# Kernel optimization log

Hardware: AMD Instinct MI355X
Metric: run time of the kernel (lower is better)

## Reference

```python
import jax, jax.numpy as jnp
import numpy as np

TEMPERATURE = 1.0


def setup_inputs() -> dict:
    key = jax.random.key(0)
    k1, k2, k3, k4, k5 = jax.random.split(key, 5)
    B, S, F = 4, 2048, 2048   # batch, seq, in_features
    E, r, O = 8, 16, 2048     # experts, lora rank, out_features
    x = jax.random.normal(k1, (B, S, F), dtype=jnp.float32)
    protos = jax.random.normal(k2, (E, F), dtype=jnp.float32)
    protos = protos / (jnp.linalg.norm(protos, axis=-1, keepdims=True) + 1e-8)  # unit prototypes (top singular vecs)
    A_stack = jax.random.normal(k3, (E, r, F), dtype=jnp.float32) * 0.02
    B_stack = jax.random.normal(k4, (E, O, r), dtype=jnp.float32) * 0.02
    scales = jax.random.uniform(k5, (E,), dtype=jnp.float32)
    return {"x": x, "prototypes": protos, "A_stack": A_stack,
            "B_stack": B_stack, "scales": scales, "top_k": 2}


def reference(x, prototypes, A_stack, B_stack, scales, top_k):
    B, S, F = x.shape
    tok = x.reshape(-1, F)                       # [t, F]
    t = tok.shape[0]
    # 1) |cosine| similarity to prototypes (protos are unit norm)
    sim = jnp.abs(tok @ prototypes.T)            # [t, E]
    # 2) top-k selection, softmax over selected (others -inf)
    top_v, idx = jax.lax.top_k(sim, top_k)       # [t, k]
    full_score = jnp.full(sim.shape, -jnp.inf, dtype=sim.dtype)
    full_score = full_score.at[jnp.arange(t)[:, None], idx].set(top_v)
    coeff = jax.nn.softmax(full_score / TEMPERATURE, axis=1)   # [t, E]
    # 3-5) per-expert LoRA deltas, scaled, then coefficient-weighted sum
    z = jnp.einsum('tf,erf->ter', tok, A_stack)                # [t, E, r]
    y = jnp.einsum('ter,eor->teo', z, B_stack)                 # [t, E, O]
    y = y * scales[None, :, None]
    delta_flat = jnp.einsum('te,teo->to', coeff, y)            # [t, O]
    # 6) dropout is identity in eval mode
    return delta_flat.reshape(B, S, -1)
```

## Files before the change

### kernel.cpp

```cpp
#include <hip/hip_runtime.h>
#include <hip/hip_bf16.h>

typedef unsigned short u16;
typedef __bf16 bf16x8 __attribute__((ext_vector_type(8)));
typedef float f32x4 __attribute__((ext_vector_type(4)));

#define T_TOTAL 8192
#define F_DIM   2048
#define E_NUM   8
#define R_RANK  16
#define ER_DIM  128
#define O_DIM   2048

__device__ __forceinline__ u16 f2bf(float f) {
  return __builtin_bit_cast(u16, (__bf16)f);
}

__global__ __launch_bounds__(256) void prep_kernel(
    const float* __restrict__ A, const float* __restrict__ Bst,
    u16* __restrict__ Abf, u16* __restrict__ BbfT) {
  const int i = blockIdx.x * 256 + threadIdx.x;
  Abf[i] = f2bf(A[i]);
  const int o = i >> 7, er = i & 127, e = er >> 4, j = er & 15;
  BbfT[i] = f2bf(Bst[e * (O_DIM * R_RANK) + o * R_RANK + j]);
}

__global__ __launch_bounds__(256) void gemm1_kernel(
    const float* __restrict__ x, const float* __restrict__ protos,
    const float* __restrict__ scales, const u16* __restrict__ Abf,
    u16* __restrict__ zc) {
  __shared__ u16 xs[16 * 136];
  __shared__ u16 as_[128 * 136];
  __shared__ float pk[8 * 128];
  __shared__ float sim_lds[16][8];
  __shared__ float w_lds[16][8];

  const int tid  = threadIdx.x;
  const int t0   = blockIdx.x * 16;
  const int row  = tid >> 4;
  const int seg  = tid & 15;
  const int lane = tid & 63;
  const int wave = tid >> 6;
  const int g    = lane >> 4;
  const int lm   = lane & 15;

  float sacc[E_NUM];
#pragma unroll
  for (int e = 0; e < E_NUM; ++e) sacc[e] = 0.f;

  const f32x4 z4 = {0.f, 0.f, 0.f, 0.f};
  f32x4 acc[2];
  acc[0] = z4; acc[1] = z4;

  for (int kt = 0; kt < F_DIM / 128; ++kt) {
    const int kb = kt * 128;
    __syncthreads();

    f32x4 xv[2];
    const float* xp = x + (size_t)(t0 + row) * F_DIM + kb + seg * 4;
    xv[0] = *reinterpret_cast<const f32x4*>(xp);
    xv[1] = *reinterpret_cast<const f32x4*>(xp + 64);

    {
      const int pe = tid >> 5;
      const int pj = (tid & 31) * 4;
      *reinterpret_cast<f32x4*>(&pk[pe * 128 + pj]) =
          *reinterpret_cast<const f32x4*>(protos + (size_t)pe * F_DIM + kb + pj);
    }

#pragma unroll
    for (int it = 0; it < 8; ++it) {
      const int c  = it * 256 + tid;
      const int er = c >> 4;
      const int ks = (c & 15) * 8;
      *reinterpret_cast<uint4*>(&as_[er * 136 + ks]) =
          *reinterpret_cast<const uint4*>(Abf + (size_t)er * F_DIM + kb + ks);
    }

#pragma unroll
    for (int p = 0; p < 2; ++p) {
      ushort4 h;
      h.x = f2bf(xv[p][0]); h.y = f2bf(xv[p][1]);
      h.z = f2bf(xv[p][2]); h.w = f2bf(xv[p][3]);
      *reinterpret_cast<ushort4*>(&xs[row * 136 + seg * 4 + p * 64]) = h;
    }
    __syncthreads();

#pragma unroll
    for (int p = 0; p < 2; ++p) {
#pragma unroll
      for (int e = 0; e < E_NUM; ++e) {
        f32x4 pv = *reinterpret_cast<const f32x4*>(&pk[e * 128 + seg * 4 + p * 64]);
        sacc[e] += xv[p][0] * pv[0] + xv[p][1] * pv[1] +
                   xv[p][2] * pv[2] + xv[p][3] * pv[3];
      }
    }

#pragma unroll
    for (int kk = 0; kk < 4; ++kk) {
      bf16x8 av = *reinterpret_cast<const bf16x8*>(&xs[lm * 136 + kk * 32 + g * 8]);
#pragma unroll
      for (int n = 0; n < 2; ++n) {
        bf16x8 bv = *reinterpret_cast<const bf16x8*>(
            &as_[(wave * 32 + n * 16 + lm) * 136 + kk * 32 + g * 8]);
        acc[n] = __builtin_amdgcn_mfma_f32_16x16x32_bf16(av, bv, acc[n], 0, 0, 0);
      }
    }
  }

#pragma unroll
  for (int s = 1; s < 16; s <<= 1)
#pragma unroll
    for (int e = 0; e < E_NUM; ++e)
      sacc[e] += __shfl_xor(sacc[e], s);
  if (seg < E_NUM) sim_lds[row][seg] = sacc[seg];
  __syncthreads();

  if (tid < 16) {
    float sv[E_NUM];
#pragma unroll
    for (int e = 0; e < E_NUM; ++e) sv[e] = fabsf(sim_lds[tid][e]);
    int e0 = 0; float b0 = sv[0];
#pragma unroll
    for (int e = 1; e < E_NUM; ++e) if (sv[e] > b0) { b0 = sv[e]; e0 = e; }
    int e1 = -1; float b1 = -3.0e38f;
#pragma unroll
    for (int e = 0; e < E_NUM; ++e) if (e != e0 && sv[e] > b1) { b1 = sv[e]; e1 = e; }
    const float d  = expf(b1 - b0);
    const float c0 = 1.f / (1.f + d);
    const float c1 = d * c0;
#pragma unroll
    for (int e = 0; e < E_NUM; ++e) w_lds[tid][e] = 0.f;
    w_lds[tid][e0] = c0 * scales[e0];
    w_lds[tid][e1] = c1 * scales[e1];
  }
  __syncthreads();

#pragma unroll
  for (int n = 0; n < 2; ++n) {
    const int er = wave * 32 + n * 16 + lm;
    const int e  = er >> 4;
#pragma unroll
    for (int i = 0; i < 4; ++i) {
      const int tl = g * 4 + i;
      zc[(size_t)(t0 + tl) * ER_DIM + er] = f2bf(acc[n][i] * w_lds[tl][e]);
    }
  }
}

__global__ __launch_bounds__(256) void gemm2_kernel(
    const u16* __restrict__ zc, const u16* __restrict__ BbfT,
    float* __restrict__ out) {
  __shared__ u16 zcs[128 * 136];
  __shared__ u16 bbs[64 * 136];

  const int tid  = threadIdx.x;
  const int o0   = blockIdx.x * 64;
  const int t0   = blockIdx.y * 128;
  const int lane = tid & 63;
  const int wave = tid >> 6;
  const int wm   = wave >> 1;
  const int wn   = wave & 1;
  const int g    = lane >> 4;
  const int lm   = lane & 15;

#pragma unroll
  for (int it = 0; it < 8; ++it) {
    const int c = it * 256 + tid;
    const int r = c >> 4;
    const int ks = (c & 15) * 8;
    *reinterpret_cast<uint4*>(&zcs[r * 136 + ks]) =
        *reinterpret_cast<const uint4*>(zc + (size_t)(t0 + r) * ER_DIM + ks);
  }
#pragma unroll
  for (int it = 0; it < 4; ++it) {
    const int c = it * 256 + tid;
    const int r = c >> 4;
    const int ks = (c & 15) * 8;
    *reinterpret_cast<uint4*>(&bbs[r * 136 + ks]) =
        *reinterpret_cast<const uint4*>(BbfT + (size_t)(o0 + r) * ER_DIM + ks);
  }
  __syncthreads();

  const f32x4 z4 = {0.f, 0.f, 0.f, 0.f};
  f32x4 acc[4][2];
#pragma unroll
  for (int m = 0; m < 4; ++m)
#pragma unroll
    for (int n = 0; n < 2; ++n) acc[m][n] = z4;

#pragma unroll
  for (int kk = 0; kk < 4; ++kk) {
    bf16x8 av[4], bv[2];
#pragma unroll
    for (int m = 0; m < 4; ++m)
      av[m] = *reinterpret_cast<const bf16x8*>(
          &zcs[(wm * 64 + m * 16 + lm) * 136 + kk * 32 + g * 8]);
#pragma unroll
    for (int n = 0; n < 2; ++n)
      bv[n] = *reinterpret_cast<const bf16x8*>(
          &bbs[(wn * 32 + n * 16 + lm) * 136 + kk * 32 + g * 8]);
#pragma unroll
    for (int m = 0; m < 4; ++m)
#pragma unroll
      for (int n = 0; n < 2; ++n)
        acc[m][n] = __builtin_amdgcn_mfma_f32_16x16x32_bf16(av[m], bv[n], acc[m][n], 0, 0, 0);
  }

#pragma unroll
  for (int m = 0; m < 4; ++m) {
#pragma unroll
    for (int n = 0; n < 2; ++n) {
      const int o = o0 + wn * 32 + n * 16 + lm;
#pragma unroll
      for (int i = 0; i < 4; ++i) {
        const int t = t0 + wm * 64 + m * 16 + g * 4 + i;
        out[(size_t)t * O_DIM + o] = acc[m][n][i];
      }
    }
  }
}

extern "C" void kernel_launch(void* const* d_in, const int* in_sizes, int n_in,
                              void* d_out, int out_size, void* d_ws, size_t ws_size,
                              hipStream_t stream) {
  const float* x      = (const float*)d_in[0];
  const float* protos = (const float*)d_in[1];
  const float* A      = (const float*)d_in[2];
  const float* Bst    = (const float*)d_in[3];
  const float* scales = (const float*)d_in[4];

  u16* zcw  = (u16*)d_ws;
  u16* Abf  = zcw + (size_t)T_TOTAL * ER_DIM;
  u16* BbfT = Abf + (size_t)ER_DIM * F_DIM;
  float* out = (float*)d_out;

  prep_kernel<<<(ER_DIM * F_DIM) / 256, 256, 0, stream>>>(A, Bst, Abf, BbfT);
  gemm1_kernel<<<T_TOTAL / 16, 256, 0, stream>>>(x, protos, scales, Abf, zcw);
  gemm2_kernel<<<dim3(O_DIM / 64, T_TOTAL / 128), 256, 0, stream>>>(zcw, BbfT, out);
}
```

Before: 175.5 us.

## Fuse routing, down-projection and up-projection into one kernel with MFMA-packed weights

Merges gemm1 and gemm2 into one kernel. Each block keeps its 16 tokens' coefficient-weighted z in LDS with an XOR swizzle and loops over all 2048 outputs, so the zc round trip through global memory and the extra launch go away. Weights are pre-packed into the per-lane MFMA fragment order, so operands are read straight from global memory without staging through LDS or barriers in the K loop. x is converted to bf16 in registers and protos are read directly. The cost is heavier direct global and L2 traffic per block, with no LDS reuse and occupancy capped by launch bounds, in exchange for fewer syncs and no intermediate tensor.

```diff
diff --git a/kernel.cpp b/kernel.cpp
--- a/kernel.cpp
+++ b/kernel.cpp
@@ -7,103 +7,95 @@
 
 #define T_TOTAL 8192
 #define F_DIM   2048
+#define O_DIM   2048
 #define E_NUM   8
-#define R_RANK  16
-#define ER_DIM  128
-#define O_DIM   2048
 
 __device__ __forceinline__ u16 f2bf(float f) {
   return __builtin_bit_cast(u16, (__bf16)f);
 }
+__device__ __forceinline__ unsigned pack2(float a, float b) {
+  return (unsigned)f2bf(a) | ((unsigned)f2bf(b) << 16);
+}
+__device__ __forceinline__ bf16x8 packbf8(f32x4 v0, f32x4 v1) {
+  uint4 hv;
+  hv.x = pack2(v0[0], v0[1]); hv.y = pack2(v0[2], v0[3]);
+  hv.z = pack2(v1[0], v1[1]); hv.w = pack2(v1[2], v1[3]);
+  return __builtin_bit_cast(bf16x8, hv);
+}
 
 __global__ __launch_bounds__(256) void prep_kernel(
     const float* __restrict__ A, const float* __restrict__ Bst,
-    u16* __restrict__ Abf, u16* __restrict__ BbfT) {
-  const int i = blockIdx.x * 256 + threadIdx.x;
-  Abf[i] = f2bf(A[i]);
-  const int o = i >> 7, er = i & 127, e = er >> 4, j = er & 15;
-  BbfT[i] = f2bf(Bst[e * (O_DIM * R_RANK) + o * R_RANK + j]);
+    u16* __restrict__ Apack, u16* __restrict__ Bpack) {
+  const int i  = blockIdx.x * 256 + threadIdx.x;
+  const int j  = i & 7;
+  const int l  = (i >> 3) & 63;
+  const int kk = (i >> 9) & 3;
+  const int s  = (i >> 11) & 7;
+  const int t  = i >> 14;
+  const int lm = l & 15, g = l >> 4;
+  {
+    const int er = s * 16 + lm;
+    const int k  = t * 128 + kk * 32 + g * 8 + j;
+    Apack[i] = f2bf(A[er * F_DIM + k]);
+  }
+  {
+    const int o  = t * 128 + s * 16 + lm;
+    const int er = kk * 32 + g * 8 + j;
+    Bpack[i] = f2bf(Bst[(er >> 4) * (O_DIM * 16) + o * 16 + (er & 15)]);
+  }
 }
 
-__global__ __launch_bounds__(256) void gemm1_kernel(
+__global__ __launch_bounds__(256, 2) void fused_kernel(
     const float* __restrict__ x, const float* __restrict__ protos,
-    const float* __restrict__ scales, const u16* __restrict__ Abf,
-    u16* __restrict__ zc) {
-  __shared__ u16 xs[16 * 136];
-  __shared__ u16 as_[128 * 136];
-  __shared__ float pk[8 * 128];
+    const float* __restrict__ scales, const u16* __restrict__ Apack,
+    const u16* __restrict__ Bpack, float* __restrict__ out) {
   __shared__ float sim_lds[16][8];
   __shared__ float w_lds[16][8];
+  __shared__ u16  zc_lds[16 * 128];
 
   const int tid  = threadIdx.x;
   const int t0   = blockIdx.x * 16;
   const int row  = tid >> 4;
   const int seg  = tid & 15;
   const int lane = tid & 63;
-  const int wave = tid >> 6;
+  const int w    = tid >> 6;
   const int g    = lane >> 4;
   const int lm   = lane & 15;
 
   float sacc[E_NUM];
 #pragma unroll
   for (int e = 0; e < E_NUM; ++e) sacc[e] = 0.f;
+  const f32x4 z4 = {0.f, 0.f, 0.f, 0.f};
+  f32x4 acc1[2];
+  acc1[0] = z4; acc1[1] = z4;
 
-  const f32x4 z4 = {0.f, 0.f, 0.f, 0.f};
-  f32x4 acc[2];
-  acc[0] = z4; acc[1] = z4;
+  const float* xs_ptr = x + (size_t)(t0 + row) * F_DIM + seg * 8;
+  const float* xf_ptr = x + (size_t)(t0 + lm) * F_DIM;
 
-  for (int kt = 0; kt < F_DIM / 128; ++kt) {
+#pragma unroll 2
+  for (int kt = 0; kt < 16; ++kt) {
     const int kb = kt * 128;
-    __syncthreads();
-
-    f32x4 xv[2];
-    const float* xp = x + (size_t)(t0 + row) * F_DIM + kb + seg * 4;
-    xv[0] = *reinterpret_cast<const f32x4*>(xp);
-    xv[1] = *reinterpret_cast<const f32x4*>(xp + 64);
-
-    {
-      const int pe = tid >> 5;
-      const int pj = (tid & 31) * 4;
-      *reinterpret_cast<f32x4*>(&pk[pe * 128 + pj]) =
-          *reinterpret_cast<const f32x4*>(protos + (size_t)pe * F_DIM + kb + pj);
+    f32x4 a0 = *reinterpret_cast<const f32x4*>(xs_ptr + kb);
+    f32x4 a1 = *reinterpret_cast<const f32x4*>(xs_ptr + kb + 4);
+#pragma unroll
+    for (int e = 0; e < E_NUM; ++e) {
+      const float* pp = protos + e * F_DIM + kb + seg * 8;
+      f32x4 p0 = *reinterpret_cast<const f32x4*>(pp);
+      f32x4 p1 = *reinterpret_cast<const f32x4*>(pp + 4);
+      sacc[e] += a0[0]*p0[0] + a0[1]*p0[1] + a0[2]*p0[2] + a0[3]*p0[3]
+               + a1[0]*p1[0] + a1[1]*p1[1] + a1[2]*p1[2] + a1[3]*p1[3];
     }
-
-#pragma unroll
-    for (int it = 0; it < 8; ++it) {
-      const int c  = it * 256 + tid;
-      const int er = c >> 4;
-      const int ks = (c & 15) * 8;
-      *reinterpret_cast<uint4*>(&as_[er * 136 + ks]) =
-          *reinterpret_cast<const uint4*>(Abf + (size_t)er * F_DIM + kb + ks);
-    }
-
-#pragma unroll
-    for (int p = 0; p < 2; ++p) {
-      ushort4 h;
-      h.x = f2bf(xv[p][0]); h.y = f2bf(xv[p][1]);
-      h.z = f2bf(xv[p][2]); h.w = f2bf(xv[p][3]);
-      *reinterpret_cast<ushort4*>(&xs[row * 136 + seg * 4 + p * 64]) = h;
-    }
-    __syncthreads();
-
-#pragma unroll
-    for (int p = 0; p < 2; ++p) {
-#pragma unroll
-      for (int e = 0; e < E_NUM; ++e) {
-        f32x4 pv = *reinterpret_cast<const f32x4*>(&pk[e * 128 + seg * 4 + p * 64]);
-        sacc[e] += xv[p][0] * pv[0] + xv[p][1] * pv[1] +
-                   xv[p][2] * pv[2] + xv[p][3] * pv[3];
-      }
-    }
-
 #pragma unroll
     for (int kk = 0; kk < 4; ++kk) {
-      bf16x8 av = *reinterpret_cast<const bf16x8*>(&xs[lm * 136 + kk * 32 + g * 8]);
+      const float* xf = xf_ptr + kb + kk * 32 + g * 8;
+      f32x4 v0 = *reinterpret_cast<const f32x4*>(xf);
+      f32x4 v1 = *reinterpret_cast<const f32x4*>(xf + 4);
+      bf16x8 av = packbf8(v0, v1);
 #pragma unroll
       for (int n = 0; n < 2; ++n) {
         bf16x8 bv = *reinterpret_cast<const bf16x8*>(
-            &as_[(wave * 32 + n * 16 + lm) * 136 + kk * 32 + g * 8]);
-        acc[n] = __builtin_amdgcn_mfma_f32_16x16x32_bf16(av, bv, acc[n], 0, 0, 0);
+            Apack + ((((size_t)kt * 8 + (w * 2 + n)) * 4 + kk) * 64 + lane) * 8);
+        acc1[n] = __builtin_amdgcn_mfma_f32_16x16x32_bf16(av, bv, acc1[n], 0, 0, 0);
       }
     }
   }
@@ -111,8 +103,7 @@
 #pragma unroll
   for (int s = 1; s < 16; s <<= 1)
 #pragma unroll
-    for (int e = 0; e < E_NUM; ++e)
-      sacc[e] += __shfl_xor(sacc[e], s);
+    for (int e = 0; e < E_NUM; ++e) sacc[e] += __shfl_xor(sacc[e], s);
   if (seg < E_NUM) sim_lds[row][seg] = sacc[seg];
   __syncthreads();
 
@@ -126,7 +117,7 @@
     int e1 = -1; float b1 = -3.0e38f;
 #pragma unroll
     for (int e = 0; e < E_NUM; ++e) if (e != e0 && sv[e] > b1) { b1 = sv[e]; e1 = e; }
-    const float d  = expf(b1 - b0);
+    const float d  = __expf(b1 - b0);
     const float c0 = 1.f / (1.f + d);
     const float c1 = d * c0;
 #pragma unroll
@@ -138,85 +129,41 @@
 
 #pragma unroll
   for (int n = 0; n < 2; ++n) {
-    const int er = wave * 32 + n * 16 + lm;
-    const int e  = er >> 4;
+    const int s2 = w * 2 + n;
 #pragma unroll
     for (int i = 0; i < 4; ++i) {
-      const int tl = g * 4 + i;
-      zc[(size_t)(t0 + tl) * ER_DIM + er] = f2bf(acc[n][i] * w_lds[tl][e]);
+      const int t = g * 4 + i;
+      zc_lds[t * 128 + ((s2 * 16 + lm) ^ ((t & 7) << 3))] =
+          f2bf(acc1[n][i] * w_lds[t][s2]);
     }
-  }
-}
-
-__global__ __launch_bounds__(256) void gemm2_kernel(
-    const u16* __restrict__ zc, const u16* __restrict__ BbfT,
-    float* __restrict__ out) {
-  __shared__ u16 zcs[128 * 136];
-  __shared__ u16 bbs[64 * 136];
-
-  const int tid  = threadIdx.x;
-  const int o0   = blockIdx.x * 64;
-  const int t0   = blockIdx.y * 128;
-  const int lane = tid & 63;
-  const int wave = tid >> 6;
-  const int wm   = wave >> 1;
-  const int wn   = wave & 1;
-  const int g    = lane >> 4;
-  const int lm   = lane & 15;
-
-#pragma unroll
-  for (int it = 0; it < 8; ++it) {
-    const int c = it * 256 + tid;
-    const int r = c >> 4;
-    const int ks = (c & 15) * 8;
-    *reinterpret_cast<uint4*>(&zcs[r * 136 + ks]) =
-        *reinterpret_cast<const uint4*>(zc + (size_t)(t0 + r) * ER_DIM + ks);
-  }
-#pragma unroll
-  for (int it = 0; it < 4; ++it) {
-    const int c = it * 256 + tid;
-    const int r = c >> 4;
-    const int ks = (c & 15) * 8;
-    *reinterpret_cast<uint4*>(&bbs[r * 136 + ks]) =
-        *reinterpret_cast<const uint4*>(BbfT + (size_t)(o0 + r) * ER_DIM + ks);
   }
   __syncthreads();
 
-  const f32x4 z4 = {0.f, 0.f, 0.f, 0.f};
-  f32x4 acc[4][2];
+  bf16x8 av2[4];
 #pragma unroll
-  for (int m = 0; m < 4; ++m)
+  for (int kk = 0; kk < 4; ++kk)
+    av2[kk] = *reinterpret_cast<const bf16x8*>(
+        &zc_lds[lm * 128 + ((kk * 32 + g * 8) ^ ((lm & 7) << 3))]);
+
+#pragma unroll 2
+  for (int ot = 0; ot < 16; ++ot) {
+    f32x4 acc2[2];
+    acc2[0] = z4; acc2[1] = z4;
 #pragma unroll
-    for (int n = 0; n < 2; ++n) acc[m][n] = z4;
-
+    for (int kk = 0; kk < 4; ++kk) {
 #pragma unroll
-  for (int kk = 0; kk < 4; ++kk) {
-    bf16x8 av[4], bv[2];
-#pragma unroll
-    for (int m = 0; m < 4; ++m)
-      av[m] = *reinterpret_cast<const bf16x8*>(
-          &zcs[(wm * 64 + m * 16 + lm) * 136 + kk * 32 + g * 8]);
-#pragma unroll
-    for (int n = 0; n < 2; ++n)
-      bv[n] = *reinterpret_cast<const bf16x8*>(
-          &bbs[(wn * 32 + n * 16 + lm) * 136 + kk * 32 + g * 8]);
-#pragma unroll
-    for (int m = 0; m < 4; ++m)
-#pragma unroll
-      for (int n = 0; n < 2; ++n)
-        acc[m][n] = __builtin_amdgcn_mfma_f32_16x16x32_bf16(av[m], bv[n], acc[m][n], 0, 0, 0);
-  }
-
-#pragma unroll
-  for (int m = 0; m < 4; ++m) {
+      for (int n = 0; n < 2; ++n) {
+        bf16x8 bv = *reinterpret_cast<const bf16x8*>(
+            Bpack + ((((size_t)ot * 8 + (w * 2 + n)) * 4 + kk) * 64 + lane) * 8);
+        acc2[n] = __builtin_amdgcn_mfma_f32_16x16x32_bf16(av2[kk], bv, acc2[n], 0, 0, 0);
+      }
+    }
 #pragma unroll
     for (int n = 0; n < 2; ++n) {
-      const int o = o0 + wn * 32 + n * 16 + lm;
+      const int o = ot * 128 + (w * 2 + n) * 16 + lm;
 #pragma unroll
-      for (int i = 0; i < 4; ++i) {
-        const int t = t0 + wm * 64 + m * 16 + g * 4 + i;
-        out[(size_t)t * O_DIM + o] = acc[m][n][i];
-      }
+      for (int i = 0; i < 4; ++i)
+        out[(size_t)(t0 + g * 4 + i) * O_DIM + o] = acc2[n][i];
     }
   }
 }
@@ -230,12 +177,10 @@
   const float* Bst    = (const float*)d_in[3];
   const float* scales = (const float*)d_in[4];
 
-  u16* zcw  = (u16*)d_ws;
-  u16* Abf  = zcw + (size_t)T_TOTAL * ER_DIM;
-  u16* BbfT = Abf + (size_t)ER_DIM * F_DIM;
+  u16* Apack = (u16*)d_ws;
+  u16* Bpack = Apack + (size_t)128 * F_DIM;
   float* out = (float*)d_out;
 
-  prep_kernel<<<(ER_DIM * F_DIM) / 256, 256, 0, stream>>>(A, Bst, Abf, BbfT);
-  gemm1_kernel<<<T_TOTAL / 16, 256, 0, stream>>>(x, protos, scales, Abf, zcw);
-  gemm2_kernel<<<dim3(O_DIM / 64, T_TOTAL / 128), 256, 0, stream>>>(zcw, BbfT, out);
+  prep_kernel<<<(128 * F_DIM) / 256, 256, 0, stream>>>(A, Bst, Apack, Bpack);
+  fused_kernel<<<T_TOTAL / 16, 256, 0, stream>>>(x, protos, scales, Apack, Bpack, out);
 }
```

Result: slower. 198.9 us (+13.3%).
